# Kernel tuning notes

Measured on AMD Instinct MI355X. Metric: run time of the kernel, lower is better.

## Reference

```python
import jax, jax.numpy as jnp
import numpy as np

N = 100000      # nodes_num
H = 256         # n_hid
E = 3200000     # edges (avg degree 32)
OUT = 2         # GATConv out_feats, num_heads = 1
NEG_SLOPE = 0.2 # DGL GATConv default leaky_relu slope


def setup_inputs() -> dict:
    key = jax.random.key(0)
    ks = jax.random.split(key, 8)
    return {
        "input": jax.random.normal(ks[0], (N, H), dtype=jnp.float32),
        "x": jax.random.normal(ks[1], (N, 1), dtype=jnp.float32),  # the torch.randn inside forward, made deterministic
        "degree": jnp.ones((N, 1), dtype=jnp.float32),             # unused by forward, kept for signature fidelity
        "edge_src": jax.random.randint(ks[2], (E,), 0, N, dtype=jnp.int32),
        "edge_dst": jax.random.randint(ks[3], (E,), 0, N, dtype=jnp.int32),
        "W": jax.random.normal(ks[4], (H, OUT), dtype=jnp.float32) * (1.0 / np.sqrt(H)),
        "attn_l": jax.random.normal(ks[5], (OUT,), dtype=jnp.float32),
        "attn_r": jax.random.normal(ks[6], (OUT,), dtype=jnp.float32),
        "bias": jax.random.normal(ks[7], (OUT,), dtype=jnp.float32) * 0.02,
    }


def _gat_conv(feat, edge_src, edge_dst, W, attn_l, attn_r, bias):
    # DGL GATConv, num_heads=1. feat: [N,H] -> [N,OUT]
    z = feat @ W                              # [N, OUT]
    el = z @ attn_l                           # [N] source term
    er = z @ attn_r                           # [N] dest term
    e = jax.nn.leaky_relu(el[edge_src] + er[edge_dst], NEG_SLOPE)  # [E]
    # edge softmax grouped by destination node (numerically stable)
    m = jax.ops.segment_max(e, edge_dst, num_segments=N)           # [N]
    ex = jnp.exp(e - m[edge_dst])                                  # [E]
    denom = jax.ops.segment_sum(ex, edge_dst, num_segments=N)      # [N]
    alpha = ex / denom[edge_dst]                                   # [E]
    out = jax.ops.segment_sum(alpha[:, None] * z[edge_src], edge_dst, num_segments=N)
    return out + bias                         # [N, OUT]


def reference(input, x, degree, edge_src, edge_dst, W, attn_l, attn_r, bias):
    coff = _gat_conv(input, edge_src, edge_dst, W, attn_l, attn_r, bias)  # [N, 2]
    # torch: mean over heads dim (num_heads=1) is identity
    std = jax.nn.relu(coff[:, 0:1])   # [N,1]
    mean = jax.nn.relu(coff[:, 1:2])  # [N,1]
    # y = ones, so y*mean == mean
    return input * jax.nn.sigmoid(x * std + mean)
```

## Files before the change

### kernel.cpp

```cpp
#include <hip/hip_runtime.h>
#include <hip/hip_fp16.h>
#include <math.h>

#define HDIM 256
#define NEG_SLOPE 0.2f


#define BSHIFT 7
#define BMASK 127
#define MAXBKT 1024

__device__ __forceinline__ float leaky(float v) {
    return v >= 0.0f ? v : NEG_SLOPE * v;
}

__device__ __forceinline__ unsigned enc_f32(float f) {
    unsigned b = __float_as_uint(f);
    return b ^ ((b >> 31) ? 0xFFFFFFFFu : 0x80000000u);
}
__device__ __forceinline__ float dec_f32(unsigned u) {
    u ^= ((u >> 31) ? 0x80000000u : 0xFFFFFFFFu);
    return __uint_as_float(u);
}

__global__ void k_node(const float* __restrict__ input,
                       const float* __restrict__ W,
                       const float* __restrict__ attn_l,
                       const float* __restrict__ attn_r,
                       float4* __restrict__ nodeinfo,
                       float* __restrict__ el_arr,
                       float* __restrict__ er_arr,
                       int n)
{
    int node = blockIdx.x * 4 + (threadIdx.x >> 6);
    int lane = threadIdx.x & 63;
    if (node >= n) return;

    const float4* inrow = (const float4*)(input + (size_t)node * HDIM);
    float4 v = inrow[lane];
    const float4* Wv = (const float4*)W;
    float4 w0 = Wv[2 * lane];
    float4 w1 = Wv[2 * lane + 1];
    float s0 = v.x * w0.x + v.y * w0.z + v.z * w1.x + v.w * w1.z;
    float s1 = v.x * w0.y + v.y * w0.w + v.z * w1.y + v.w * w1.w;

    #pragma unroll
    for (int off = 32; off > 0; off >>= 1) {
        s0 += __shfl_xor(s0, off);
        s1 += __shfl_xor(s1, off);
    }

    if (lane == 0) {
        float el = s0 * attn_l[0] + s1 * attn_l[1];
        float er = s0 * attn_r[0] + s1 * attn_r[1];
        nodeinfo[node] = make_float4(el, er, s0, s1);
        el_arr[node] = el;
        er_arr[node] = er;
    }
}

__global__ void k_maxel(const float* __restrict__ el, unsigned* __restrict__ M_enc, int n)
{
    float m = -1e30f;
    for (int i = blockIdx.x * blockDim.x + threadIdx.x; i < n;
         i += gridDim.x * blockDim.x)
        m = fmaxf(m, el[i]);
    #pragma unroll
    for (int off = 32; off > 0; off >>= 1)
        m = fmaxf(m, __shfl_xor(m, off));
    __shared__ float s[4];
    int lane = threadIdx.x & 63, w = threadIdx.x >> 6;
    if (lane == 0) s[w] = m;
    __syncthreads();
    if (threadIdx.x == 0) {
        float mm = fmaxf(fmaxf(s[0], s[1]), fmaxf(s[2], s[3]));
        atomicMax(M_enc, enc_f32(mm));
    }
}

__global__ void k_bin(const int* __restrict__ src,
                      const int* __restrict__ dst,
                      unsigned* __restrict__ cursor,
                      unsigned* __restrict__ edgebuf,
                      const float4* __restrict__ nodeinfo,
                      const float* __restrict__ er_arr,
                      const unsigned* __restrict__ M_enc,
                      unsigned* __restrict__ num,
                      float* __restrict__ denom,
                      int e, int nbkt, int cap)
{
    __shared__ unsigned h1[MAXBKT];
    __shared__ unsigned h2[MAXBKT];
    for (int t = threadIdx.x; t < nbkt; t += blockDim.x) { h1[t] = 0u; h2[t] = 0u; }
    __syncthreads();

    int chunk = (e + gridDim.x - 1) / gridDim.x;
    int lo = blockIdx.x * chunk;
    int hi = min(e, lo + chunk);

    for (int i = lo + (int)threadIdx.x; i < hi; i += blockDim.x)
        atomicAdd(&h1[dst[i] >> BSHIFT], 1u);
    __syncthreads();

    for (int t = threadIdx.x; t < nbkt; t += blockDim.x) {
        unsigned c = h1[t];
        h1[t] = c ? atomicAdd(&cursor[t], c) : 0u;
    }
    __syncthreads();

    for (int i = lo + (int)threadIdx.x; i < hi; i += blockDim.x) {
        int d = dst[i];
        int b = d >> BSHIFT;
        unsigned r = h1[b] + atomicAdd(&h2[b], 1u);
        int s = src[i];
        if (r < (unsigned)cap) {
            edgebuf[(size_t)b * cap + r] = ((unsigned)s << BSHIFT) | (unsigned)(d & BMASK);
        } else {
            float Mel = dec_f32(*M_enc);
            float4 ns = nodeinfo[s];
            float erd = er_arr[d];
            float ex = __expf(leaky(ns.x + erd) - leaky(Mel + erd));
            __half2 h = __floats2half2_rn(ex * ns.z, ex * ns.w);
            unsigned hv = *(unsigned*)&h;
            unsigned* np = num + d;
            asm volatile("global_atomic_pk_add_f16 %0, %1, off"
                         :: "v"(np), "v"(hv) : "memory");
            float* dp = denom + d;
            asm volatile("global_atomic_add_f32 %0, %1, off"
                         :: "v"(dp), "v"(ex) : "memory");
        }
    }
}

__global__ void k_proc(const unsigned* __restrict__ cursor,
                       const unsigned* __restrict__ edgebuf,
                       const float4* __restrict__ nodeinfo,
                       const float* __restrict__ er_arr,
                       const unsigned* __restrict__ M_enc,
                       const unsigned* __restrict__ num,
                       const float* __restrict__ denom,
                       const float* __restrict__ x,
                       const float* __restrict__ bias,
                       float* __restrict__ g,
                       int n, int cap)
{
    __shared__ float sD[128], s0[128], s1[128], ser[128];
    int b = blockIdx.x;
    int dbase = b << BSHIFT;
    int t = threadIdx.x;
    if (t < 128) {
        sD[t] = 0.f; s0[t] = 0.f; s1[t] = 0.f;
        int d = dbase + t;
        ser[t] = (d < n) ? er_arr[d] : 0.f;
    }
    __syncthreads();

    float Mel = dec_f32(*M_enc);
    unsigned cnt = cursor[b];
    if (cnt > (unsigned)cap) cnt = (unsigned)cap;
    const unsigned* buf = edgebuf + (size_t)b * cap;

    for (unsigned i = (unsigned)t; i < cnt; i += blockDim.x) {
        unsigned rec = buf[i];
        int s = rec >> BSHIFT;
        int dl = rec & BMASK;
        float4 ns = nodeinfo[s];
        float erd = ser[dl];
        float ex = __expf(leaky(ns.x + erd) - leaky(Mel + erd));
        atomicAdd(&sD[dl], ex);
        atomicAdd(&s0[dl], ex * ns.z);
        atomicAdd(&s1[dl], ex * ns.w);
    }
    __syncthreads();

    if (t < 128) {
        int d = dbase + t;
        if (d < n) {
            float D = sD[t] + denom[d];
            __half2 h = *(const __half2*)(num + d);
            float2 f = __half22float2(h);
            float S0 = s0[t] + f.x;
            float S1 = s1[t] + f.y;
            float c0 = bias[0], c1 = bias[1];
            if (D > 0.f) { float inv = 1.0f / D; c0 += S0 * inv; c1 += S1 * inv; }
            float tt = x[d] * fmaxf(c0, 0.f) + fmaxf(c1, 0.f);
            g[d] = 1.0f / (1.0f + __expf(-tt));
        }
    }
}

__global__ void k_edge(const int* __restrict__ src,
                       const int* __restrict__ dst,
                       const float4* __restrict__ nodeinfo,
                       const float* __restrict__ er_arr,
                       const unsigned* __restrict__ M_enc,
                       unsigned* __restrict__ num,
                       float* __restrict__ denom,
                       int e)
{
    int i = blockIdx.x * blockDim.x + threadIdx.x;
    if (i >= e) return;
    float Mel = dec_f32(*M_enc);
    int s = src[i], d = dst[i];
    float4 ns = nodeinfo[s];
    float erd = er_arr[d];
    float ex = __expf(leaky(ns.x + erd) - leaky(Mel + erd));
    __half2 h = __floats2half2_rn(ex * ns.z, ex * ns.w);
    unsigned hv = *(unsigned*)&h;
    unsigned* np = num + d;
    asm volatile("global_atomic_pk_add_f16 %0, %1, off"
                 :: "v"(np), "v"(hv) : "memory");
    float* dp = denom + d;
    asm volatile("global_atomic_add_f32 %0, %1, off"
                 :: "v"(dp), "v"(ex) : "memory");
}

__global__ void k_reduce(const unsigned* __restrict__ num,
                         const float* __restrict__ denom,
                         const float* __restrict__ x,
                         const float* __restrict__ bias,
                         float* __restrict__ g,
                         int n)
{
    int i = blockIdx.x * blockDim.x + threadIdx.x;
    if (i >= n) return;
    float D = denom[i];
    float c0 = bias[0], c1 = bias[1];
    if (D > 0.0f) {
        __half2 h = *(const __half2*)(num + i);
        float2 f = __half22float2(h);
        float inv = 1.0f / D;
        c0 += f.x * inv;
        c1 += f.y * inv;
    }
    float t = x[i] * fmaxf(c0, 0.0f) + fmaxf(c1, 0.0f);
    g[i] = 1.0f / (1.0f + __expf(-t));
}

__global__ void k_final(const float* __restrict__ input,
                        const float* __restrict__ g,
                        float* __restrict__ out,
                        int n)
{
    int node = blockIdx.x * 4 + (threadIdx.x >> 6);
    int lane = threadIdx.x & 63;
    if (node >= n) return;
    float gg = g[node];
    const float4* inrow = (const float4*)(input + (size_t)node * HDIM);
    float4* outrow = (float4*)(out + (size_t)node * HDIM);
    float4 v = inrow[lane];
    outrow[lane] = make_float4(v.x * gg, v.y * gg, v.z * gg, v.w * gg);
}

extern "C" void kernel_launch(void* const* d_in, const int* in_sizes, int n_in,
                              void* d_out, int out_size, void* d_ws, size_t ws_size,
                              hipStream_t stream)
{
    const float* input  = (const float*)d_in[0];
    const float* x      = (const float*)d_in[1];
    const int* esrc     = (const int*)d_in[3];
    const int* edst     = (const int*)d_in[4];
    const float* W      = (const float*)d_in[5];
    const float* attn_l = (const float*)d_in[6];
    const float* attn_r = (const float*)d_in[7];
    const float* bias   = (const float*)d_in[8];
    float* out = (float*)d_out;

    const int n = in_sizes[1];
    const int e = in_sizes[3];

    char* ws = (char*)d_ws;
    unsigned* num      = (unsigned*)ws;
    float*    denom    = (float*)(ws + (size_t)4 * n);
    unsigned* M_enc    = (unsigned*)(ws + (size_t)8 * n);
    unsigned* cursor   = (unsigned*)(ws + (size_t)8 * n + 64);
    size_t    base2    = (size_t)8 * n + 64 + 4 * MAXBKT;
    float4*   nodeinfo = (float4*)(ws + base2);
    float*    el_arr   = (float*)(ws + base2 + (size_t)16 * n);
    float*    er_arr   = (float*)(ws + base2 + (size_t)20 * n);
    float*    g        = (float*)(ws + base2 + (size_t)24 * n);
    unsigned* edgebuf  = (unsigned*)(ws + base2 + (size_t)28 * n);

    const int nbkt  = (n + BMASK) >> BSHIFT;
    const int meanb = (nbkt > 0) ? e / nbkt : 0;
    const int cap   = meanb + meanb / 4 + 64;
    const size_t need_fast = base2 + (size_t)28 * n + 4ull * nbkt * cap;
    const bool fast = (nbkt <= MAXBKT) && (ws_size >= need_fast);

    hipMemsetAsync(ws, 0, (size_t)8 * n + 64 + 4 * MAXBKT, stream);

    dim3 blk(256);
    int nodeBlocks = (n + 3) / 4;
    int flatBlocks = (n + 255) / 256;

    k_node<<<nodeBlocks, blk, 0, stream>>>(input, W, attn_l, attn_r,
                                           nodeinfo, el_arr, er_arr, n);
    k_maxel<<<120, blk, 0, stream>>>(el_arr, M_enc, n);

    if (fast) {
        k_bin<<<256, blk, 0, stream>>>(esrc, edst, cursor, edgebuf,
                                       nodeinfo, er_arr, M_enc, num, denom,
                                       e, nbkt, cap);
        k_proc<<<nbkt, blk, 0, stream>>>(cursor, edgebuf, nodeinfo, er_arr, M_enc,
                                         num, denom, x, bias, g, n, cap);
    } else {
        int edgeBlocks = (e + 255) / 256;
        k_edge<<<edgeBlocks, blk, 0, stream>>>(esrc, edst, nodeinfo, er_arr, M_enc,
                                               num, denom, e);
        k_reduce<<<flatBlocks, blk, 0, stream>>>(num, denom, x, bias, g, n);
    }

    k_final<<<nodeBlocks, blk, 0, stream>>>(input, g, out, n);
}
```

Measured before the change: 387.7 us.

## Stage edges in LDS with vectorized loads and use many small binning blocks

The binning kernel now processes fixed 4096-edge chunks per block, launching about 782 blocks instead of 256. Each block loads src/dst once with int4 vector loads, packs each record and its bucket id into shared memory, and builds the histogram in the same pass. The scatter pass then reads from LDS instead of re-reading dst and src from global memory. Roughly 24KB of LDS per block may limit occupancy, and more blocks means more global cursor atomics.

```diff
diff --git a/kernel.cpp b/kernel.cpp
--- a/kernel.cpp
+++ b/kernel.cpp
@@ -9,6 +9,7 @@
 #define BSHIFT 7
 #define BMASK 127
 #define MAXBKT 1024
+#define EPB 4096
 
 __device__ __forceinline__ float leaky(float v) {
     return v >= 0.0f ? v : NEG_SLOPE * v;
@@ -78,28 +79,60 @@
     }
 }
 
-__global__ void k_bin(const int* __restrict__ src,
-                      const int* __restrict__ dst,
-                      unsigned* __restrict__ cursor,
-                      unsigned* __restrict__ edgebuf,
-                      const float4* __restrict__ nodeinfo,
-                      const float* __restrict__ er_arr,
-                      const unsigned* __restrict__ M_enc,
-                      unsigned* __restrict__ num,
-                      float* __restrict__ denom,
-                      int e, int nbkt, int cap)
+__global__ __launch_bounds__(256, 4)
+void k_bin(const int* __restrict__ src,
+           const int* __restrict__ dst,
+           unsigned* __restrict__ cursor,
+           unsigned* __restrict__ edgebuf,
+           const float4* __restrict__ nodeinfo,
+           const float* __restrict__ er_arr,
+           const unsigned* __restrict__ M_enc,
+           unsigned* __restrict__ num,
+           float* __restrict__ denom,
+           int e, int nbkt, int cap)
 {
     __shared__ unsigned h1[MAXBKT];
     __shared__ unsigned h2[MAXBKT];
+    __shared__ unsigned recs[EPB];
+    __shared__ unsigned short bkt[EPB];
+
     for (int t = threadIdx.x; t < nbkt; t += blockDim.x) { h1[t] = 0u; h2[t] = 0u; }
     __syncthreads();
 
-    int chunk = (e + gridDim.x - 1) / gridDim.x;
-    int lo = blockIdx.x * chunk;
-    int hi = min(e, lo + chunk);
-
-    for (int i = lo + (int)threadIdx.x; i < hi; i += blockDim.x)
-        atomicAdd(&h1[dst[i] >> BSHIFT], 1u);
+    int lo = blockIdx.x * EPB;
+    int cnt = min(EPB, e - lo);
+
+    if (cnt == EPB) {
+        const int4* s4 = (const int4*)(src + lo);
+        const int4* d4 = (const int4*)(dst + lo);
+        #pragma unroll
+        for (int k = 0; k < EPB / 1024; ++k) {
+            int i4 = (int)threadIdx.x + k * 256;
+            int4 sv = s4[i4];
+            int4 dv = d4[i4];
+            int i = 4 * i4;
+            recs[i + 0] = ((unsigned)sv.x << BSHIFT) | ((unsigned)dv.x & BMASK);
+            recs[i + 1] = ((unsigned)sv.y << BSHIFT) | ((unsigned)dv.y & BMASK);
+            recs[i + 2] = ((unsigned)sv.z << BSHIFT) | ((unsigned)dv.z & BMASK);
+            recs[i + 3] = ((unsigned)sv.w << BSHIFT) | ((unsigned)dv.w & BMASK);
+            bkt[i + 0] = (unsigned short)((unsigned)dv.x >> BSHIFT);
+            bkt[i + 1] = (unsigned short)((unsigned)dv.y >> BSHIFT);
+            bkt[i + 2] = (unsigned short)((unsigned)dv.z >> BSHIFT);
+            bkt[i + 3] = (unsigned short)((unsigned)dv.w >> BSHIFT);
+            atomicAdd(&h1[(unsigned)dv.x >> BSHIFT], 1u);
+            atomicAdd(&h1[(unsigned)dv.y >> BSHIFT], 1u);
+            atomicAdd(&h1[(unsigned)dv.z >> BSHIFT], 1u);
+            atomicAdd(&h1[(unsigned)dv.w >> BSHIFT], 1u);
+        }
+    } else {
+        for (int i = threadIdx.x; i < cnt; i += blockDim.x) {
+            int s = src[lo + i];
+            int d = dst[lo + i];
+            recs[i] = ((unsigned)s << BSHIFT) | ((unsigned)d & BMASK);
+            bkt[i] = (unsigned short)((unsigned)d >> BSHIFT);
+            atomicAdd(&h1[(unsigned)d >> BSHIFT], 1u);
+        }
+    }
     __syncthreads();
 
     for (int t = threadIdx.x; t < nbkt; t += blockDim.x) {
@@ -108,14 +141,15 @@
     }
     __syncthreads();
 
-    for (int i = lo + (int)threadIdx.x; i < hi; i += blockDim.x) {
-        int d = dst[i];
-        int b = d >> BSHIFT;
+    for (int i = threadIdx.x; i < cnt; i += blockDim.x) {
+        int b = (int)bkt[i];
+        unsigned rec = recs[i];
         unsigned r = h1[b] + atomicAdd(&h2[b], 1u);
-        int s = src[i];
         if (r < (unsigned)cap) {
-            edgebuf[(size_t)b * cap + r] = ((unsigned)s << BSHIFT) | (unsigned)(d & BMASK);
+            edgebuf[(size_t)b * cap + r] = rec;
         } else {
+            int s = (int)(rec >> BSHIFT);
+            int d = (b << BSHIFT) | (int)(rec & BMASK);
             float Mel = dec_f32(*M_enc);
             float4 ns = nodeinfo[s];
             float erd = er_arr[d];
@@ -298,9 +332,10 @@
     k_maxel<<<120, blk, 0, stream>>>(el_arr, M_enc, n);
 
     if (fast) {
-        k_bin<<<256, blk, 0, stream>>>(esrc, edst, cursor, edgebuf,
-                                       nodeinfo, er_arr, M_enc, num, denom,
-                                       e, nbkt, cap);
+        int binBlocks = (e + EPB - 1) / EPB;
+        k_bin<<<binBlocks, blk, 0, stream>>>(esrc, edst, cursor, edgebuf,
+                                             nodeinfo, er_arr, M_enc, num, denom,
+                                             e, nbkt, cap);
         k_proc<<<nbkt, blk, 0, stream>>>(cursor, edgebuf, nodeinfo, er_arr, M_enc,
                                          num, denom, x, bias, g, n, cap);
     } else {
```

Result: faster. 336.2 us (-13.3%).
